# Kernel optimization log

Measured on AMD Instinct MI355X. Metric: run time of the kernel, lower is better.

Reference implementation:

```python
import jax, jax.numpy as jnp
import numpy as np

NORM_EPS = 1e-6
QUANT_EPS = 1e-8


def setup_inputs() -> dict:
    key = jax.random.key(0)
    k1, k2 = jax.random.split(key)
    B, S, D_IN, D_OUT = 2, 4096, 2048, 2048
    x = jax.random.normal(k1, (B, S, D_IN), dtype=jnp.float32)
    # master fp32 weights (kaiming-uniform-ish scale)
    weight = jax.random.uniform(k2, (D_OUT, D_IN), dtype=jnp.float32,
                                minval=-1.0, maxval=1.0) * (1.0 / np.sqrt(D_IN))
    norm_weight = jnp.ones((D_IN,), dtype=jnp.float32)
    return {"x": x, "weight": weight, "norm_weight": norm_weight}


def _rmsnorm(x, gain):
    rms = jnp.sqrt(jnp.mean(x * x, axis=-1, keepdims=True) + NORM_EPS)
    return x / rms * gain


def _ternary_quantize(w):
    gamma = jnp.mean(jnp.abs(w))                       # absmean scale (scalar)
    w_q = jnp.clip(jnp.round(w / (gamma + QUANT_EPS)), -1.0, 1.0)
    return w_q, gamma


def reference(x, weight, norm_weight):
    # 1) RMSNorm input
    xn = _rmsnorm(x, norm_weight)
    # 2) ternary-quantize weights {-1,0,+1} with absmean gamma
    w_q, gamma = _ternary_quantize(weight)
    # 3) matmul with ternary weights, 4) scale by gamma
    # xn: [B,S,Din], w_q: [Dout,Din] -> [B,S,Dout]
    return jnp.einsum('bsd,od->bso', xn, w_q) * gamma
```

## Files before the change

### kernel.cpp

```cpp
#include <hip/hip_runtime.h>
#include <hip/hip_bf16.h>
#include <stdint.h>

typedef unsigned short u16;
typedef signed char i8;

#define D_INNER 2048
#define D_OUTER 2048
#define MROWS   8192
#define W_ELEMS (D_OUTER * D_INNER)
#define NPART   1024

#define BM 256
#define BN 256
#define BK 128
#define NKT (D_INNER / BK)
#define SLOT_BYTES 65536
#define LDS_TOTAL  131072

typedef __attribute__((ext_vector_type(4))) float f32x4;
typedef __attribute__((ext_vector_type(4))) int   i32x4;
typedef __attribute__((ext_vector_type(16))) int  i32x16;

__global__ __launch_bounds__(256) void prep_kernel(const float* __restrict__ x,
                            const float* __restrict__ g,
                            const float* __restrict__ w,
                            i8* __restrict__ xn, float* __restrict__ srow,
                            float* __restrict__ partials) {
  int t = threadIdx.x;
  int lane = t & 63, wvi = t >> 6;

  if (blockIdx.x >= MROWS / 4) {
    __shared__ float red[4];
    int p = blockIdx.x - MROWS / 4;
    int base = p * 1024;
    float s = 0.f;
#pragma unroll
    for (int r = 0; r < 4; ++r) {
      f32x4 v = ((const f32x4*)w)[base + r * 256 + t];
      s += fabsf(v[0]) + fabsf(v[1]) + fabsf(v[2]) + fabsf(v[3]);
    }
    for (int off = 32; off; off >>= 1) s += __shfl_down(s, off, 64);
    if (lane == 0) red[wvi] = s;
    __syncthreads();
    if (t == 0) partials[p] = red[0] + red[1] + red[2] + red[3];
    return;
  }

  int row = blockIdx.x * 4 + wvi;
  const f32x4* xr = (const f32x4*)(x + (size_t)row * D_INNER);
  const f32x4* gr = (const f32x4*)g;
  i8* xo = xn + (size_t)row * D_INNER;

  f32x4 v[8], gv[8];
#pragma unroll
  for (int r = 0; r < 8; ++r) {
    v[r]  = __builtin_nontemporal_load(&xr[lane + r * 64]);
    gv[r] = gr[lane + r * 64];
  }
  float s = 0.f, m = 0.f;
#pragma unroll
  for (int r = 0; r < 8; ++r) {
    s += v[r][0]*v[r][0] + v[r][1]*v[r][1] + v[r][2]*v[r][2] + v[r][3]*v[r][3];
    m = fmaxf(m, fmaxf(fmaxf(fabsf(v[r][0]*gv[r][0]), fabsf(v[r][1]*gv[r][1])),
                       fmaxf(fabsf(v[r][2]*gv[r][2]), fabsf(v[r][3]*gv[r][3]))));
  }
#pragma unroll
  for (int off = 32; off; off >>= 1) {
    s += __shfl_xor(s, off, 64);
    m = fmaxf(m, __shfl_xor(m, off, 64));
  }
  float invr = 1.0f / sqrtf(s * (1.0f / (float)D_INNER) + 1e-6f);
  float amax = fmaxf(m * invr, 1e-12f);
  float step = amax * (1.0f / 127.0f);
  float qs   = 127.0f / amax;
  if (lane == 0) srow[row] = step;

#pragma unroll
  for (int r = 0; r < 8; ++r) {
    char4 q;
    float qv;
    qv = fminf(127.f, fmaxf(-127.f, rintf(v[r][0]*invr*gv[r][0]*qs))); q.x = (i8)(int)qv;
    qv = fminf(127.f, fmaxf(-127.f, rintf(v[r][1]*invr*gv[r][1]*qs))); q.y = (i8)(int)qv;
    qv = fminf(127.f, fmaxf(-127.f, rintf(v[r][2]*invr*gv[r][2]*qs))); q.z = (i8)(int)qv;
    qv = fminf(127.f, fmaxf(-127.f, rintf(v[r][3]*invr*gv[r][3]*qs))); q.w = (i8)(int)qv;
    ((char4*)xo)[lane + r * 64] = q;
  }
}

__global__ __launch_bounds__(256) void quant_kernel(const float* __restrict__ w,
                             const float* __restrict__ partials,
                             float* __restrict__ gamma_out, i8* __restrict__ wq) {
  f32x4 pv = ((const f32x4*)partials)[threadIdx.x];
  double d = (double)pv[0] + (double)pv[1] + (double)pv[2] + (double)pv[3];
  for (int off = 32; off; off >>= 1) d += __shfl_down(d, off, 64);
  __shared__ double red[4];
  int lane = threadIdx.x & 63, wvi = threadIdx.x >> 6;
  if (lane == 0) red[wvi] = d;
  __syncthreads();
  double total = red[0] + red[1] + red[2] + red[3];
  float gamma = (float)(total * (1.0 / (double)W_ELEMS));
  float inv = 1.0f / (gamma + 1e-8f);
  if (blockIdx.x == 0 && threadIdx.x == 0) *gamma_out = gamma;

  int tid = blockIdx.x * blockDim.x + threadIdx.x;
  int stride = gridDim.x * blockDim.x;
  for (int i = tid; i < W_ELEMS / 4; i += stride) {
    f32x4 v = ((const f32x4*)w)[i];
    char4 q;
    q.x = (i8)(int)fminf(1.f, fmaxf(-1.f, rintf(v[0] * inv)));
    q.y = (i8)(int)fminf(1.f, fmaxf(-1.f, rintf(v[1] * inv)));
    q.z = (i8)(int)fminf(1.f, fmaxf(-1.f, rintf(v[2] * inv)));
    q.w = (i8)(int)fminf(1.f, fmaxf(-1.f, rintf(v[3] * inv)));
    ((char4*)wq)[i] = q;
  }
}

#define GLDS(SRC, DST) __builtin_amdgcn_global_load_lds( \
    (const __attribute__((address_space(1))) void*)(SRC), \
    (__attribute__((address_space(3))) void*)(DST), 16, 0, 0)
#define WAITVM(N) asm volatile("s_waitcnt vmcnt(" #N ")")
#define BAR()     __builtin_amdgcn_s_barrier()
#define FENCE()   __builtin_amdgcn_sched_barrier(0)

__global__ __launch_bounds__(512, 2) void gemm_bt(const i8* __restrict__ A,
                                                  const i8* __restrict__ Bw,
                                                  const float* __restrict__ gamma_p,
                                                  const float* __restrict__ srow,
                                                  float* __restrict__ C) {
  extern __shared__ i8 lds[];

  int f   = blockIdx.y * 8 + blockIdx.x;
  int xcd = f & 7;
  int gg  = f >> 3;
  int orig = xcd * 32 + gg;
  int nb  = orig & 7;
  int mb  = orig >> 3;
  int bm0 = mb * BM;
  int bn0 = nb * BN;

  int tid  = threadIdx.x;
  int lane = tid & 63;
  int wv   = tid >> 6;
  int wr   = wv >> 2;
  int wc   = wv & 3;
  int l31  = lane & 31;
  int hi   = lane >> 5;

  const i8* Ag = A  + (size_t)bm0 * D_INNER;
  const i8* Bg = Bw + (size_t)bn0 * D_INNER;

  size_t src0 = (size_t)(tid >> 3) * D_INNER + (((tid & 7) ^ ((tid >> 3) & 7)) << 4);
  int dst0 = tid * 16;

  int rdA = (wr * 128 + l31) * BK;
  int rdB[2];
  rdB[0] = 32768 + (wc * 64 +      l31) * BK;
  rdB[1] = 32768 + (wc * 64 + 32 + l31) * BK;
  int swz[4];
#pragma unroll
  for (int ks = 0; ks < 4; ++ks)
    swz[ks] = (((ks << 1) | hi) ^ (l31 & 7)) << 4;

  i32x16 acc[4][2] = {};

#define STAGE_FULL(T_, S_) do { \
    _Pragma("unroll") for (int r = 0; r < 4; ++r) \
      GLDS(Ag + src0 + (size_t)r * (64 * D_INNER) + (size_t)(T_) * BK, \
           lds + (S_) * SLOT_BYTES + r * 8192 + dst0); \
    _Pragma("unroll") for (int r = 0; r < 4; ++r) \
      GLDS(Bg + src0 + (size_t)r * (64 * D_INNER) + (size_t)(T_) * BK, \
           lds + (S_) * SLOT_BYTES + 32768 + r * 8192 + dst0); \
  } while (0)

#define COMPUTE(T_) do { \
    const i8* sl_ = lds + ((T_) & 1) * SLOT_BYTES; \
    i32x4 bf_[4][2]; \
    _Pragma("unroll") for (int ks = 0; ks < 4; ++ks) \
      _Pragma("unroll") for (int nj = 0; nj < 2; ++nj) \
        bf_[ks][nj] = *(const i32x4*)(sl_ + rdB[nj] + swz[ks]); \
    _Pragma("unroll") for (int ph = 0; ph < 4; ++ph) { \
      i32x4 af_[4]; \
      _Pragma("unroll") for (int ks = 0; ks < 4; ++ks) \
        af_[ks] = *(const i32x4*)(sl_ + rdA + ph * 4096 + swz[ks]); \
      __builtin_amdgcn_s_setprio(1); \
      _Pragma("unroll") for (int ks = 0; ks < 4; ++ks) { \
        acc[ph][0] = __builtin_amdgcn_mfma_i32_32x32x32_i8(af_[ks], bf_[ks][0], acc[ph][0], 0, 0, 0); \
        acc[ph][1] = __builtin_amdgcn_mfma_i32_32x32x32_i8(af_[ks], bf_[ks][1], acc[ph][1], 0, 0, 0); \
      } \
      __builtin_amdgcn_s_setprio(0); \
    } \
  } while (0)

#define TILE(T_, DO_STAGE, WAITSTMT) do { \
    FENCE(); \
    BAR();                        \
    FENCE(); \
    if (DO_STAGE) STAGE_FULL((T_) + 1, ((T_) + 1) & 1); \
    FENCE(); \
    WAITSTMT;                     \
    FENCE(); \
    BAR();                        \
    FENCE(); \
    COMPUTE(T_); \
  } while (0)

  STAGE_FULL(0, 0);

  for (int t = 0; t < NKT - 1; ++t)
    TILE(t, 1, WAITVM(8));
  TILE(NKT - 1, 0, WAITVM(0));

  float gamma = *gamma_p;
  int colb = bn0 + wc * 64 + l31;
#pragma unroll
  for (int mi = 0; mi < 4; ++mi) {
    int rbase = bm0 + wr * 128 + mi * 32 + hi * 4;
    f32x4 sg[4];
#pragma unroll
    for (int q = 0; q < 4; ++q) {
      f32x4 sv = *(const f32x4*)(srow + rbase + q * 8);
      sg[q] = sv * gamma;
    }
#pragma unroll
    for (int nj = 0; nj < 2; ++nj) {
      i32x16 v = acc[mi][nj];
      float* cp = C + (size_t)rbase * D_OUTER + (colb + nj * 32);
#pragma unroll
      for (int q = 0; q < 4; ++q)
#pragma unroll
        for (int rr = 0; rr < 4; ++rr)
          cp[(size_t)(q * 8 + rr) * D_OUTER] = (float)v[q * 4 + rr] * sg[q][rr];
    }
  }
}

extern "C" void kernel_launch(void* const* d_in, const int* in_sizes, int n_in,
                              void* d_out, int out_size, void* d_ws, size_t ws_size,
                              hipStream_t stream) {
  const float* x = (const float*)d_in[0];
  const float* w = (const float*)d_in[1];
  const float* g = (const float*)d_in[2];
  float* out = (float*)d_out;

  float* gamma_p  = (float*)d_ws;
  float* partials = (float*)((char*)d_ws + 64);
  float* srow     = (float*)((char*)d_ws + 8192);
  i8* xn = (i8*)((char*)d_ws + 8192 + 32768);
  i8* wq = (i8*)((char*)d_ws + 8192 + 32768 + (size_t)MROWS * D_INNER);

  static bool attr_set = false;
  if (!attr_set) {
    (void)hipFuncSetAttribute(reinterpret_cast<const void*>(&gemm_bt),
                              hipFuncAttributeMaxDynamicSharedMemorySize, LDS_TOTAL);
    attr_set = true;
  }

  prep_kernel<<<MROWS / 4 + NPART, 256, 0, stream>>>(x, g, w, xn, srow, partials);
  quant_kernel<<<2048, 256, 0, stream>>>(w, partials, gamma_p, wq);
  gemm_bt<<<dim3(8, 32), 512, LDS_TOTAL, stream>>>(xn, wq, gamma_p, srow, out);
}
```

Before: 164.7 us.

## Use 4-wave 256x256 GEMM tiles with loads interleaved across MFMA phases

Cuts the GEMM workgroup from 8 waves to 4. Each wave now computes a 128x128 sub-tile with a 4x4 accumulator grid, which raises register reuse of the A and B fragments loaded from LDS. The next tile's global-to-LDS loads are split across the first three compute phases so they overlap with the MFMAs, and each K step needs only one barrier instead of two. In exchange, each wave's accumulators take 256 registers and fewer waves are resident to hide latency. The code also waits for all outstanding loads (vmcnt 0) at the top of every iteration.

```diff
diff --git a/kernel.cpp b/kernel.cpp
--- a/kernel.cpp
+++ b/kernel.cpp
@@ -123,7 +123,7 @@
 #define BAR()     __builtin_amdgcn_s_barrier()
 #define FENCE()   __builtin_amdgcn_sched_barrier(0)
 
-__global__ __launch_bounds__(512, 2) void gemm_bt(const i8* __restrict__ A,
+__global__ __launch_bounds__(256, 1) void gemm_bt(const i8* __restrict__ A,
                                                   const i8* __restrict__ Bw,
                                                   const float* __restrict__ gamma_p,
                                                   const float* __restrict__ srow,
@@ -142,77 +142,76 @@
   int tid  = threadIdx.x;
   int lane = tid & 63;
   int wv   = tid >> 6;
-  int wr   = wv >> 2;
-  int wc   = wv & 3;
+  int wr   = wv >> 1;
+  int wc   = wv & 1;
   int l31  = lane & 31;
   int hi   = lane >> 5;
 
   const i8* Ag = A  + (size_t)bm0 * D_INNER;
   const i8* Bg = Bw + (size_t)bn0 * D_INNER;
 
-  size_t src0 = (size_t)(tid >> 3) * D_INNER + (((tid & 7) ^ ((tid >> 3) & 7)) << 4);
-  int dst0 = tid * 16;
+  size_t srcx = (size_t)(tid >> 3) * D_INNER + (((tid & 7) ^ ((tid >> 3) & 7)) << 4);
 
   int rdA = (wr * 128 + l31) * BK;
-  int rdB[2];
-  rdB[0] = 32768 + (wc * 64 +      l31) * BK;
-  rdB[1] = 32768 + (wc * 64 + 32 + l31) * BK;
+  int rdB = 32768 + (wc * 128 + l31) * BK;
   int swz[4];
 #pragma unroll
   for (int ks = 0; ks < 4; ++ks)
     swz[ks] = (((ks << 1) | hi) ^ (l31 & 7)) << 4;
 
-  i32x16 acc[4][2] = {};
-
-#define STAGE_FULL(T_, S_) do { \
-    _Pragma("unroll") for (int r = 0; r < 4; ++r) \
-      GLDS(Ag + src0 + (size_t)r * (64 * D_INNER) + (size_t)(T_) * BK, \
-           lds + (S_) * SLOT_BYTES + r * 8192 + dst0); \
-    _Pragma("unroll") for (int r = 0; r < 4; ++r) \
-      GLDS(Bg + src0 + (size_t)r * (64 * D_INNER) + (size_t)(T_) * BK, \
-           lds + (S_) * SLOT_BYTES + 32768 + r * 8192 + dst0); \
+  i32x16 acc[4][4] = {};
+  i32x4 bf_[4][4];
+
+#define GLDS_A(T_, RR, S_) \
+    GLDS(Ag + srcx + (size_t)(RR) * (32 * D_INNER) + (size_t)(T_) * BK, \
+         lds + (S_) * SLOT_BYTES + (RR) * 4096 + tid * 16)
+#define GLDS_B(T_, RR, S_) \
+    GLDS(Bg + srcx + (size_t)(RR) * (32 * D_INNER) + (size_t)(T_) * BK, \
+         lds + (S_) * SLOT_BYTES + 32768 + (RR) * 4096 + tid * 16)
+
+#define PHASE(T_, P_, DS_) do { \
+    if (DS_) { \
+      if ((P_) == 0) { GLDS_A(T_+1, 0, (T_+1)&1); GLDS_A(T_+1, 1, (T_+1)&1); \
+                       GLDS_A(T_+1, 2, (T_+1)&1); GLDS_B(T_+1, 0, (T_+1)&1); \
+                       GLDS_B(T_+1, 1, (T_+1)&1); GLDS_B(T_+1, 2, (T_+1)&1); } \
+      if ((P_) == 1) { GLDS_A(T_+1, 3, (T_+1)&1); GLDS_A(T_+1, 4, (T_+1)&1); \
+                       GLDS_A(T_+1, 5, (T_+1)&1); GLDS_B(T_+1, 3, (T_+1)&1); \
+                       GLDS_B(T_+1, 4, (T_+1)&1); GLDS_B(T_+1, 5, (T_+1)&1); } \
+      if ((P_) == 2) { GLDS_A(T_+1, 6, (T_+1)&1); GLDS_A(T_+1, 7, (T_+1)&1); \
+                       GLDS_B(T_+1, 6, (T_+1)&1); GLDS_B(T_+1, 7, (T_+1)&1); } \
+    } \
+    const i8* sl_ = lds + ((T_) & 1) * SLOT_BYTES; \
+    if ((P_) == 0) { \
+      _Pragma("unroll") for (int ks = 0; ks < 4; ++ks) \
+        _Pragma("unroll") for (int nj = 0; nj < 4; ++nj) \
+          bf_[ks][nj] = *(const i32x4*)(sl_ + rdB + nj * 4096 + swz[ks]); \
+    } \
+    i32x4 af_[4]; \
+    _Pragma("unroll") for (int ks = 0; ks < 4; ++ks) \
+      af_[ks] = *(const i32x4*)(sl_ + rdA + (P_) * 4096 + swz[ks]); \
+    __builtin_amdgcn_s_setprio(1); \
+    _Pragma("unroll") for (int ks = 0; ks < 4; ++ks) \
+      _Pragma("unroll") for (int nj = 0; nj < 4; ++nj) \
+        acc[P_][nj] = __builtin_amdgcn_mfma_i32_32x32x32_i8(af_[ks], bf_[ks][nj], acc[P_][nj], 0, 0, 0); \
+    __builtin_amdgcn_s_setprio(0); \
   } while (0)
 
-#define COMPUTE(T_) do { \
-    const i8* sl_ = lds + ((T_) & 1) * SLOT_BYTES; \
-    i32x4 bf_[4][2]; \
-    _Pragma("unroll") for (int ks = 0; ks < 4; ++ks) \
-      _Pragma("unroll") for (int nj = 0; nj < 2; ++nj) \
-        bf_[ks][nj] = *(const i32x4*)(sl_ + rdB[nj] + swz[ks]); \
-    _Pragma("unroll") for (int ph = 0; ph < 4; ++ph) { \
-      i32x4 af_[4]; \
-      _Pragma("unroll") for (int ks = 0; ks < 4; ++ks) \
-        af_[ks] = *(const i32x4*)(sl_ + rdA + ph * 4096 + swz[ks]); \
-      __builtin_amdgcn_s_setprio(1); \
-      _Pragma("unroll") for (int ks = 0; ks < 4; ++ks) { \
-        acc[ph][0] = __builtin_amdgcn_mfma_i32_32x32x32_i8(af_[ks], bf_[ks][0], acc[ph][0], 0, 0, 0); \
-        acc[ph][1] = __builtin_amdgcn_mfma_i32_32x32x32_i8(af_[ks], bf_[ks][1], acc[ph][1], 0, 0, 0); \
-      } \
-      __builtin_amdgcn_s_setprio(0); \
-    } \
-  } while (0)
-
-#define TILE(T_, DO_STAGE, WAITSTMT) do { \
-    FENCE(); \
-    BAR();                        \
-    FENCE(); \
-    if (DO_STAGE) STAGE_FULL((T_) + 1, ((T_) + 1) & 1); \
-    FENCE(); \
-    WAITSTMT;                     \
-    FENCE(); \
-    BAR();                        \
-    FENCE(); \
-    COMPUTE(T_); \
-  } while (0)
-
-  STAGE_FULL(0, 0);
-
-  for (int t = 0; t < NKT - 1; ++t)
-    TILE(t, 1, WAITVM(8));
-  TILE(NKT - 1, 0, WAITVM(0));
+#pragma unroll
+  for (int rr = 0; rr < 8; ++rr) { GLDS_A(0, rr, 0); GLDS_B(0, rr, 0); }
+
+  for (int t = 0; t < NKT; ++t) {
+    WAITVM(0);
+    FENCE();
+    BAR();
+    FENCE();
+    if (t < NKT - 1) {
+      PHASE(t, 0, 1); PHASE(t, 1, 1); PHASE(t, 2, 1); PHASE(t, 3, 1);
+    } else {
+      PHASE(t, 0, 0); PHASE(t, 1, 0); PHASE(t, 2, 0); PHASE(t, 3, 0);
+    }
+  }
 
   float gamma = *gamma_p;
-  int colb = bn0 + wc * 64 + l31;
 #pragma unroll
   for (int mi = 0; mi < 4; ++mi) {
     int rbase = bm0 + wr * 128 + mi * 32 + hi * 4;
@@ -223,9 +222,10 @@
       sg[q] = sv * gamma;
     }
 #pragma unroll
-    for (int nj = 0; nj < 2; ++nj) {
+    for (int nj = 0; nj < 4; ++nj) {
+      int colb = bn0 + wc * 128 + nj * 32 + l31;
       i32x16 v = acc[mi][nj];
-      float* cp = C + (size_t)rbase * D_OUTER + (colb + nj * 32);
+      float* cp = C + (size_t)rbase * D_OUTER + colb;
 #pragma unroll
       for (int q = 0; q < 4; ++q)
 #pragma unroll
@@ -258,5 +258,5 @@
 
   prep_kernel<<<MROWS / 4 + NPART, 256, 0, stream>>>(x, g, w, xn, srow, partials);
   quant_kernel<<<2048, 256, 0, stream>>>(w, partials, gamma_p, wq);
-  gemm_bt<<<dim3(8, 32), 512, LDS_TOTAL, stream>>>(xn, wq, gamma_p, srow, out);
-}
+  gemm_bt<<<dim3(8, 32), 256, LDS_TOTAL, stream>>>(xn, wq, gamma_p, srow, out);
+}
```

After: 161.9 us. Within noise of the previous version (-1.7%).
